# Kernel optimization log

Hardware: AMD Instinct MI355X
Metric: run time of the kernel (lower is better)

## Reference

```python
import jax, jax.numpy as jnp
import numpy as np

TOP_K = 2
EPS = 1e-6

def setup_inputs() -> dict:
    key = jax.random.key(0)
    ks = jax.random.split(key, 6)
    Bt, S, D, E, R = 4, 4096, 1024, 8, 4
    s = lambda d: 1.0 / np.sqrt(d)
    return {
        "x": jax.random.normal(ks[0], (Bt, S, D), jnp.float32),
        "W_base": jax.random.normal(ks[1], (D, D), jnp.float32) * s(D),
        "b_base": jax.random.normal(ks[2], (D,), jnp.float32) * 0.02,
        "W_router": jax.random.normal(ks[3], (E, D), jnp.float32) * s(D),
        "A": jax.random.normal(ks[4], (E, D, R), jnp.float32) * s(D),
        "B": jax.random.normal(ks[5], (E, R, D), jnp.float32) * s(R),
    }

def reference(x, W_base, b_base, W_router, A, B):
    # frozen base linear: [b,s,d] @ [out,d]^T + bias
    base_out = jnp.einsum('bsd,od->bso', x, W_base) + b_base
    # router softmax gate over experts
    logits = jnp.einsum('bsd,ed->bse', x, W_router)
    gate = jax.nn.softmax(logits, axis=-1)
    # top-k scatter-mask (values kept are the gate values themselves)
    topv, topi = jax.lax.top_k(gate, TOP_K)                    # [b,s,k]
    mask = jnp.sum(jax.nn.one_hot(topi, gate.shape[-1], dtype=gate.dtype), axis=-2)
    gate = gate * mask
    gate = gate / (jnp.sum(gate, axis=-1, keepdims=True) + EPS)
    # batched rank-4 LoRA experts, gating applied in low-rank space
    h = jnp.einsum('bsd,edr->bser', x, A)                      # [b,s,E,r]
    hg = h * gate[..., None]                                   # weight before up-proj
    lora_out = jnp.einsum('bser,ero->bso', hg, B)
    return base_out + lora_out
```

## Files before the change

kernel.cpp:

```cpp
#include <hip/hip_runtime.h>
#include <cstdint>

typedef __attribute__((ext_vector_type(8))) short short8;
typedef __attribute__((ext_vector_type(4))) float f32x4;

__device__ inline unsigned short f2bf(float f){
  union { float f; uint32_t u; } v; v.f = f;
  uint32_t r = v.u + 0x7FFFu + ((v.u >> 16) & 1u);
  return (unsigned short)(r >> 16);
}

#define GLL(gp, lp) __builtin_amdgcn_global_load_lds(              \
    (const __attribute__((address_space(1))) void*)(gp),           \
    (__attribute__((address_space(3))) void*)(lp), 16, 0, 0)

#define DSRO(dst, addr, off) \
  asm volatile("ds_read_b128 %0, %1 offset:" off : "=v"(dst) : "v"(addr))

__global__ __launch_bounds__(256) void kconv(const float* __restrict__ W,
                                             const float* __restrict__ A,
                                             const float* __restrict__ Bm,
                                             unsigned short* __restrict__ Wb,
                                             unsigned short* __restrict__ BTt,
                                             unsigned short* __restrict__ W2b){
  int i = blockIdx.x * 256 + threadIdx.x;
  Wb[i] = f2bf(W[i]);
  if (i < 32768){
    int o = i >> 5, c = i & 31;
    BTt[i] = f2bf(Bm[(size_t)c*1024 + o]);
    int n = i >> 10, d = i & 1023;
    W2b[i] = f2bf(A[(((size_t)(n>>2))*1024 + d)*4 + (n&3)]);
  }
}

__global__ __launch_bounds__(256) void kxl2(const float* __restrict__ x,
                                            const float* __restrict__ Wr,
                                            unsigned short* __restrict__ xb,
                                            float* __restrict__ gate){
  __shared__ float wr[8192];
  const int tid  = threadIdx.x;
  const int lane = tid & 63;
  const int wid  = tid >> 6;
  {
    const float4* s  = (const float4*)Wr;
    float4*       d4 = (float4*)wr;
    #pragma unroll
    for (int j=0;j<8;j++) d4[j*256+tid] = s[j*256+tid];
  }
  __syncthreads();
  const int tk  = lane >> 3, ln8 = lane & 7;
  const size_t tok = (size_t)blockIdx.x*32 + wid*8 + tk;
  const float4* xr = (const float4*)(x + tok*1024);
  ushort4*      xd = (ushort4*)(xb + tok*1024);
  const float4* wv = (const float4*)wr;
  float p[8] = {0.f,0.f,0.f,0.f,0.f,0.f,0.f,0.f};
  #pragma unroll 4
  for (int it=0; it<32; it++){
    float4 v = xr[it*8 + ln8];
    ushort4 o; o.x=f2bf(v.x); o.y=f2bf(v.y); o.z=f2bf(v.z); o.w=f2bf(v.w);
    xd[it*8 + ln8] = o;
    #pragma unroll
    for (int e=0;e<8;e++){
      float4 wq = wv[e*256 + it*8 + ln8];
      p[e] += v.x*wq.x + v.y*wq.y + v.z*wq.z + v.w*wq.w;
    }
  }
  #pragma unroll
  for (int off=1; off<8; off<<=1){
    #pragma unroll
    for (int e=0;e<8;e++) p[e] += __shfl_xor(p[e], off, 64);
  }
  if (ln8 == 0){
    float mx = p[0];
    #pragma unroll
    for (int e=1;e<8;e++) mx = fmaxf(mx, p[e]);
    float ex[8], s2 = 0.f;
    #pragma unroll
    for (int e=0;e<8;e++){ ex[e] = __expf(p[e]-mx); s2 += ex[e]; }
    int i1 = 0; float v1 = ex[0];
    #pragma unroll
    for (int e=1;e<8;e++) if (ex[e] > v1){ v1 = ex[e]; i1 = e; }
    int i2 = -1; float v2 = -1.f;
    #pragma unroll
    for (int e=0;e<8;e++) if (e != i1 && ex[e] > v2){ v2 = ex[e]; i2 = e; }
    float g1 = v1/s2, g2 = v2/s2;
    float rs = 1.f/(g1 + g2 + 1e-6f);
    float* go = gate + tok*8;
    #pragma unroll
    for (int e=0;e<8;e++) go[e] = (e==i1 ? g1 : (e==i2 ? g2 : 0.f)) * rs;
  }
}

__global__ __launch_bounds__(512, 2) void kgemm6(const unsigned short* __restrict__ xb,
                                                 const unsigned short* __restrict__ Wb,
                                                 const unsigned short* __restrict__ BTt,
                                                 const unsigned short* __restrict__ W2b,
                                                 const float* __restrict__ gate,
                                                 const float* __restrict__ bias,
                                                 float* __restrict__ out){
  __shared__ __attribute__((aligned(128))) char lds[131072];
  char* ldsc = lds;
  const uint32_t L = (uint32_t)(uintptr_t)lds;
  const int tid  = threadIdx.x;
  const int lane = tid & 63;
  const int w    = tid >> 6;
  const int mblk = blockIdx.x & 63;
  const int nblk = blockIdx.x >> 6;
  const int m0 = mblk << 8, n0 = nblk << 8;
  const int wm = w >> 2, wn = w & 3;
  const int lrow = lane & 15;
  const int q    = lane >> 4;

  const int swzk = (lrow & 7) << 4;
  const uint32_t vA0 = L + (uint32_t)(wm*128 + lrow)*128 + (uint32_t)((q<<4) ^ swzk);
  const uint32_t vA1 = L + (uint32_t)(wm*128 + lrow)*128 + (uint32_t)(((q^4)<<4) ^ swzk);
  const uint32_t vB0 = L + 65536u + (uint32_t)(wn*64 + lrow)*128 + (uint32_t)((q<<4) ^ swzk);
  const uint32_t vB1 = L + 65536u + (uint32_t)(wn*64 + lrow)*128 + (uint32_t)(((q^4)<<4) ^ swzk);

  const int rowL = lane >> 3;
  const int colb = ((lane & 7) ^ rowL) << 4;
  const int rbA = (w>>2)*128 + (w&3)*16;
  const int rbB = (w>>1)*64 + (w&1)*16;
  const char* Ag = (const char*)xb + ((size_t)(m0 + rbA + rowL) << 11) + colb;
  const char* Bg = (const char*)Wb + ((size_t)(n0 + rbB + rowL) << 11) + colb;

#define STG_A(tt, h, ss) do{                                                    \
    GLL(Ag + (size_t)(h)*131072 + (tt)*128,                                     \
        ldsc + (ss)*32768 + (rbA + (h)*64)*128 + lane*16);                      \
    GLL(Ag + (size_t)(h)*131072 + 16384 + (tt)*128,                             \
        ldsc + (ss)*32768 + (rbA + (h)*64 + 8)*128 + lane*16); }while(0)
#define STG_B(tt, h, ss) do{                                                    \
    GLL(Bg + (size_t)(h)*65536 + (tt)*128,                                      \
        ldsc + 65536 + (ss)*32768 + (rbB + (h)*32)*128 + lane*16);              \
    GLL(Bg + (size_t)(h)*65536 + 16384 + (tt)*128,                              \
        ldsc + 65536 + (ss)*32768 + (rbB + (h)*32 + 8)*128 + lane*16); }while(0)

  f32x4 acc[8][4];
  #pragma unroll
  for (int a2=0;a2<8;a2++)
    #pragma unroll
    for (int b2=0;b2<4;b2++) acc[a2][b2] = (f32x4){0.f,0.f,0.f,0.f};
  f32x4 acc_h[4];
  #pragma unroll
  for (int f=0; f<4; f++) acc_h[f] = (f32x4){0.f,0.f,0.f,0.f};

  const unsigned short* c2p = W2b + (size_t)((wn&1)*16 + lrow)*1024 + q*8;

  STG_A(0,0,0); STG_A(0,1,0); STG_B(0,0,0); STG_B(0,1,0);
  asm volatile("s_waitcnt vmcnt(0)" ::: "memory");
  __builtin_amdgcn_s_barrier();

  short8 a[8], b0[4], b1[4];
  #pragma unroll 1
  for (int t = 0; t < 16; ++t){
    const int s = t & 1, sn = s ^ 1;
    const uint32_t va0 = vA0 + s*32768, va1 = vA1 + s*32768;
    const uint32_t vb0 = vB0 + s*32768, vb1 = vB1 + s*32768;
    short8 c2[2];
    c2[0] = *(const short8*)(c2p + t*64);
    c2[1] = *(const short8*)(c2p + t*64 + 32);
    DSRO(a[0], va0, "0");    DSRO(a[1], va1, "0");
    DSRO(a[2], va0, "2048"); DSRO(a[3], va1, "2048");
    DSRO(a[4], va0, "4096"); DSRO(a[5], va1, "4096");
    DSRO(a[6], va0, "6144"); DSRO(a[7], va1, "6144");
    DSRO(b0[0], vb0, "0");    DSRO(b0[1], vb1, "0");
    DSRO(b0[2], vb0, "2048"); DSRO(b0[3], vb1, "2048");
    if (t < 15){ STG_A(t+1, 0, sn); asm volatile("s_waitcnt vmcnt(2)" ::: "memory"); }
    else       {                    asm volatile("s_waitcnt vmcnt(0)" ::: "memory"); }
    __builtin_amdgcn_s_barrier();
    asm volatile("s_waitcnt lgkmcnt(0)" ::: "memory");
    __builtin_amdgcn_sched_barrier(0);
    __builtin_amdgcn_s_setprio(1);
    #pragma unroll
    for (int kk=0;kk<2;kk++)
      #pragma unroll
      for (int fm=0;fm<4;fm++)
        #pragma unroll
        for (int fn=0;fn<2;fn++)
          acc[fm][fn] = __builtin_amdgcn_mfma_f32_16x16x32_bf16(a[fm*2+kk], b0[fn*2+kk], acc[fm][fn], 0, 0, 0);
    __builtin_amdgcn_s_setprio(0);
    __builtin_amdgcn_s_barrier();
    DSRO(b1[0], vb0, "4096"); DSRO(b1[1], vb1, "4096");
    DSRO(b1[2], vb0, "6144"); DSRO(b1[3], vb1, "6144");
    if (t < 15) STG_A(t+1, 1, sn);
    __builtin_amdgcn_s_barrier();
    asm volatile("s_waitcnt lgkmcnt(0)" ::: "memory");
    __builtin_amdgcn_sched_barrier(0);
    __builtin_amdgcn_s_setprio(1);
    #pragma unroll
    for (int kk=0;kk<2;kk++)
      #pragma unroll
      for (int fm=0;fm<4;fm++)
        #pragma unroll
        for (int fn=0;fn<2;fn++)
          acc[fm][2+fn] = __builtin_amdgcn_mfma_f32_16x16x32_bf16(a[fm*2+kk], b1[fn*2+kk], acc[fm][2+fn], 0, 0, 0);
    if (wn < 2){
      #pragma unroll
      for (int kk=0;kk<2;kk++)
        #pragma unroll
        for (int f=0;f<4;f++)
          acc_h[f] = __builtin_amdgcn_mfma_f32_16x16x32_bf16(a[f*2+kk], c2[kk], acc_h[f], 0, 0, 0);
    }
    __builtin_amdgcn_s_setprio(0);
    __builtin_amdgcn_s_barrier();
    DSRO(a[0], va0, "8192");  DSRO(a[1], va1, "8192");
    DSRO(a[2], va0, "10240"); DSRO(a[3], va1, "10240");
    DSRO(a[4], va0, "12288"); DSRO(a[5], va1, "12288");
    DSRO(a[6], va0, "14336"); DSRO(a[7], va1, "14336");
    if (t < 15) STG_B(t+1, 0, sn);
    __builtin_amdgcn_s_barrier();
    asm volatile("s_waitcnt lgkmcnt(0)" ::: "memory");
    __builtin_amdgcn_sched_barrier(0);
    __builtin_amdgcn_s_setprio(1);
    #pragma unroll
    for (int kk=0;kk<2;kk++)
      #pragma unroll
      for (int fm=0;fm<4;fm++)
        #pragma unroll
        for (int fn=0;fn<2;fn++)
          acc[4+fm][2+fn] = __builtin_amdgcn_mfma_f32_16x16x32_bf16(a[fm*2+kk], b1[fn*2+kk], acc[4+fm][2+fn], 0, 0, 0);
    __builtin_amdgcn_s_setprio(0);
    __builtin_amdgcn_s_barrier();
    if (t < 15){ STG_B(t+1, 1, sn); asm volatile("s_waitcnt vmcnt(2)" ::: "memory"); }
    __builtin_amdgcn_s_barrier();
    __builtin_amdgcn_s_setprio(1);
    #pragma unroll
    for (int kk=0;kk<2;kk++)
      #pragma unroll
      for (int fm=0;fm<4;fm++)
        #pragma unroll
        for (int fn=0;fn<2;fn++)
          acc[4+fm][fn] = __builtin_amdgcn_mfma_f32_16x16x32_bf16(a[fm*2+kk], b0[fn*2+kk], acc[4+fm][fn], 0, 0, 0);
    if (wn >= 2){
      #pragma unroll
      for (int kk=0;kk<2;kk++)
        #pragma unroll
        for (int f=0;f<4;f++)
          acc_h[f] = __builtin_amdgcn_mfma_f32_16x16x32_bf16(a[f*2+kk], c2[kk], acc_h[f], 0, 0, 0);
    }
    __builtin_amdgcn_s_setprio(0);
    __builtin_amdgcn_s_barrier();
  }

  __syncthreads();
  {
    float4* gl4 = (float4*)(ldsc + 24576);
    gl4[tid] = ((const float4*)(gate + (size_t)m0*8))[tid];
  }
  __syncthreads();
  unsigned short* HGl = (unsigned short*)ldsc;
  const float*    gl  = (const float*)(ldsc + 24576);
  {
    const int rbase = wm*128 + (wn>>1)*64;
    const int n = (wn&1)*16 + lrow;
    #pragma unroll
    for (int f=0; f<4; f++)
      #pragma unroll
      for (int j=0;j<4;j++){
        int row = rbase + f*16 + q*4 + j;
        HGl[row*40 + n] = f2bf(acc_h[f][j] * gl[row*8 + (n>>2)]);
      }
  }
  __syncthreads();
  {
    short8 hb[4];
    #pragma unroll
    for (int fn=0; fn<4; fn++)
      hb[fn] = *(const short8*)(BTt + (size_t)(n0 + wn*64 + fn*16 + lrow)*32 + q*8);
    #pragma unroll
    for (int fm=0; fm<8; fm++){
      short8 ha = *(const short8*)((const char*)HGl + (size_t)(wm*128 + fm*16 + lrow)*80 + q*16);
      #pragma unroll
      for (int fn=0; fn<4; fn++)
        acc[fm][fn] = __builtin_amdgcn_mfma_f32_16x16x32_bf16(ha, hb[fn], acc[fm][fn], 0, 0, 0);
    }
  }

  #pragma unroll
  for (int fn=0;fn<4;fn++){
    int col = n0 + wn*64 + fn*16 + lrow;
    float bv = bias[col];
    #pragma unroll
    for (int fm=0;fm<8;fm++){
      int rb = m0 + wm*128 + fm*16 + q*4;
      #pragma unroll
      for (int j=0;j<4;j++)
        out[(size_t)(rb+j)*1024 + col] = acc[fm][fn][j] + bv;
    }
  }
#undef STG_A
#undef STG_B
}

extern "C" void kernel_launch(void* const* d_in, const int* in_sizes, int n_in,
                              void* d_out, int out_size, void* d_ws, size_t ws_size,
                              hipStream_t stream){
  const float* x  = (const float*)d_in[0];
  const float* W  = (const float*)d_in[1];
  const float* bb = (const float*)d_in[2];
  const float* Wr = (const float*)d_in[3];
  const float* A  = (const float*)d_in[4];
  const float* Bm = (const float*)d_in[5];
  float* out = (float*)d_out;
  char* ws = (char*)d_ws;

  unsigned short* Wb   = (unsigned short*)(ws + 0);
  unsigned short* BTt  = (unsigned short*)(ws + 2097152);
  unsigned short* W2b  = (unsigned short*)(ws + 2162688);
  float*          gate = (float*)         (ws + 2228224);
  unsigned short* xb   = (unsigned short*)(ws + 2752512);

  kconv<<<4096, 256, 0, stream>>>(W, A, Bm, Wb, BTt, W2b);
  kxl2<<<512, 256, 0, stream>>>(x, Wr, xb, gate);
  kgemm6<<<256, 512, 0, stream>>>(xb, Wb, BTt, W2b, gate, bb, out);
}
```

Measured before the change: 86.85 us.

## Prefetch LoRA down-projection fragments and overlap LDS reads with MFMA sub-phases

Replaces the synchronous per-iteration global loads of the LoRA A fragments (c2) with asm global loads issued one K-step ahead and double-buffered in registers. Each MFMA phase is split in half with a partial lgkmcnt wait, so the first MFMAs start while later ds_reads are still in flight. The vmcnt waits are adjusted to account for the extra outstanding loads. It also shrinks the LDS row stride for the gated hidden tile from 40 to 36 elements and moves the gate buffer to match. The finer waits and hand-written vmcnt counts make the schedule fragile, and the new stride could change LDS bank-conflict behaviour.

New measurement: 82.01 us. -5.6%, faster.

```diff
diff --git a/kernel.cpp b/kernel.cpp
--- a/kernel.cpp
+++ b/kernel.cpp
@@ -16,6 +16,8 @@
 
 #define DSRO(dst, addr, off) \
   asm volatile("ds_read_b128 %0, %1 offset:" off : "=v"(dst) : "v"(addr))
+#define GLD16(dst, ptr) \
+  asm volatile("global_load_dwordx4 %0, %1, off" : "=v"(dst) : "v"(ptr) : "memory")
 
 __global__ __launch_bounds__(256) void kconv(const float* __restrict__ W,
                                              const float* __restrict__ A,
@@ -145,9 +147,13 @@
   for (int f=0; f<4; f++) acc_h[f] = (f32x4){0.f,0.f,0.f,0.f};
 
   const unsigned short* c2p = W2b + (size_t)((wn&1)*16 + lrow)*1024 + q*8;
+  short8 c2cur0, c2cur1, c2nxt0, c2nxt1;
 
   STG_A(0,0,0); STG_A(0,1,0); STG_B(0,0,0); STG_B(0,1,0);
+  GLD16(c2cur0, c2p);
+  GLD16(c2cur1, c2p + 32);
   asm volatile("s_waitcnt vmcnt(0)" ::: "memory");
+  __builtin_amdgcn_sched_barrier(0);
   __builtin_amdgcn_s_barrier();
 
   short8 a[8], b0[4], b1[4];
@@ -156,50 +162,62 @@
     const int s = t & 1, sn = s ^ 1;
     const uint32_t va0 = vA0 + s*32768, va1 = vA1 + s*32768;
     const uint32_t vb0 = vB0 + s*32768, vb1 = vB1 + s*32768;
-    short8 c2[2];
-    c2[0] = *(const short8*)(c2p + t*64);
-    c2[1] = *(const short8*)(c2p + t*64 + 32);
     DSRO(a[0], va0, "0");    DSRO(a[1], va1, "0");
     DSRO(a[2], va0, "2048"); DSRO(a[3], va1, "2048");
     DSRO(a[4], va0, "4096"); DSRO(a[5], va1, "4096");
     DSRO(a[6], va0, "6144"); DSRO(a[7], va1, "6144");
+    if (t < 15){ STG_A(t+1, 0, sn); asm volatile("s_waitcnt vmcnt(2)" ::: "memory"); }
+    else       {                    asm volatile("s_waitcnt vmcnt(0)" ::: "memory"); }
+    __builtin_amdgcn_sched_barrier(0);
     DSRO(b0[0], vb0, "0");    DSRO(b0[1], vb1, "0");
     DSRO(b0[2], vb0, "2048"); DSRO(b0[3], vb1, "2048");
-    if (t < 15){ STG_A(t+1, 0, sn); asm volatile("s_waitcnt vmcnt(2)" ::: "memory"); }
-    else       {                    asm volatile("s_waitcnt vmcnt(0)" ::: "memory"); }
-    __builtin_amdgcn_s_barrier();
+    __builtin_amdgcn_s_barrier();
+    asm volatile("s_waitcnt lgkmcnt(2)" ::: "memory");
+    __builtin_amdgcn_sched_barrier(0);
+    __builtin_amdgcn_s_setprio(1);
+    #pragma unroll
+    for (int kk=0;kk<2;kk++)
+      #pragma unroll
+      for (int fm=0;fm<4;fm++)
+        acc[fm][0] = __builtin_amdgcn_mfma_f32_16x16x32_bf16(a[fm*2+kk], b0[kk], acc[fm][0], 0, 0, 0);
     asm volatile("s_waitcnt lgkmcnt(0)" ::: "memory");
     __builtin_amdgcn_sched_barrier(0);
-    __builtin_amdgcn_s_setprio(1);
-    #pragma unroll
-    for (int kk=0;kk<2;kk++)
-      #pragma unroll
-      for (int fm=0;fm<4;fm++)
-        #pragma unroll
-        for (int fn=0;fn<2;fn++)
-          acc[fm][fn] = __builtin_amdgcn_mfma_f32_16x16x32_bf16(a[fm*2+kk], b0[fn*2+kk], acc[fm][fn], 0, 0, 0);
+    #pragma unroll
+    for (int kk=0;kk<2;kk++)
+      #pragma unroll
+      for (int fm=0;fm<4;fm++)
+        acc[fm][1] = __builtin_amdgcn_mfma_f32_16x16x32_bf16(a[fm*2+kk], b0[2+kk], acc[fm][1], 0, 0, 0);
     __builtin_amdgcn_s_setprio(0);
     __builtin_amdgcn_s_barrier();
     DSRO(b1[0], vb0, "4096"); DSRO(b1[1], vb1, "4096");
     DSRO(b1[2], vb0, "6144"); DSRO(b1[3], vb1, "6144");
-    if (t < 15) STG_A(t+1, 1, sn);
-    __builtin_amdgcn_s_barrier();
+    if (t < 15){
+      STG_A(t+1, 1, sn);
+      GLD16(c2nxt0, c2p + (t+1)*64);
+      GLD16(c2nxt1, c2p + (t+1)*64 + 32);
+    }
+    __builtin_amdgcn_s_barrier();
+    asm volatile("s_waitcnt lgkmcnt(2)" ::: "memory");
+    __builtin_amdgcn_sched_barrier(0);
+    __builtin_amdgcn_s_setprio(1);
+    #pragma unroll
+    for (int kk=0;kk<2;kk++)
+      #pragma unroll
+      for (int fm=0;fm<4;fm++)
+        acc[fm][2] = __builtin_amdgcn_mfma_f32_16x16x32_bf16(a[fm*2+kk], b1[kk], acc[fm][2], 0, 0, 0);
     asm volatile("s_waitcnt lgkmcnt(0)" ::: "memory");
     __builtin_amdgcn_sched_barrier(0);
-    __builtin_amdgcn_s_setprio(1);
-    #pragma unroll
-    for (int kk=0;kk<2;kk++)
-      #pragma unroll
-      for (int fm=0;fm<4;fm++)
-        #pragma unroll
-        for (int fn=0;fn<2;fn++)
-          acc[fm][2+fn] = __builtin_amdgcn_mfma_f32_16x16x32_bf16(a[fm*2+kk], b1[fn*2+kk], acc[fm][2+fn], 0, 0, 0);
+    #pragma unroll
+    for (int kk=0;kk<2;kk++)
+      #pragma unroll
+      for (int fm=0;fm<4;fm++)
+        acc[fm][3] = __builtin_amdgcn_mfma_f32_16x16x32_bf16(a[fm*2+kk], b1[2+kk], acc[fm][3], 0, 0, 0);
     if (wn < 2){
       #pragma unroll
-      for (int kk=0;kk<2;kk++)
-        #pragma unroll
-        for (int f=0;f<4;f++)
-          acc_h[f] = __builtin_amdgcn_mfma_f32_16x16x32_bf16(a[f*2+kk], c2[kk], acc_h[f], 0, 0, 0);
+      for (int f=0;f<4;f++){
+        acc_h[f] = __builtin_amdgcn_mfma_f32_16x16x32_bf16(a[f*2],   c2cur0, acc_h[f], 0, 0, 0);
+        acc_h[f] = __builtin_amdgcn_mfma_f32_16x16x32_bf16(a[f*2+1], c2cur1, acc_h[f], 0, 0, 0);
+      }
     }
     __builtin_amdgcn_s_setprio(0);
     __builtin_amdgcn_s_barrier();
@@ -209,19 +227,32 @@
     DSRO(a[6], va0, "14336"); DSRO(a[7], va1, "14336");
     if (t < 15) STG_B(t+1, 0, sn);
     __builtin_amdgcn_s_barrier();
+    asm volatile("s_waitcnt lgkmcnt(4)" ::: "memory");
+    __builtin_amdgcn_sched_barrier(0);
+    __builtin_amdgcn_s_setprio(1);
+    #pragma unroll
+    for (int kk=0;kk<2;kk++)
+      #pragma unroll
+      for (int fm=0;fm<2;fm++)
+        #pragma unroll
+        for (int fn=0;fn<2;fn++)
+          acc[4+fm][2+fn] = __builtin_amdgcn_mfma_f32_16x16x32_bf16(a[fm*2+kk], b1[fn*2+kk], acc[4+fm][2+fn], 0, 0, 0);
     asm volatile("s_waitcnt lgkmcnt(0)" ::: "memory");
     __builtin_amdgcn_sched_barrier(0);
-    __builtin_amdgcn_s_setprio(1);
-    #pragma unroll
-    for (int kk=0;kk<2;kk++)
-      #pragma unroll
-      for (int fm=0;fm<4;fm++)
+    #pragma unroll
+    for (int kk=0;kk<2;kk++)
+      #pragma unroll
+      for (int fm=2;fm<4;fm++)
         #pragma unroll
         for (int fn=0;fn<2;fn++)
           acc[4+fm][2+fn] = __builtin_amdgcn_mfma_f32_16x16x32_bf16(a[fm*2+kk], b1[fn*2+kk], acc[4+fm][2+fn], 0, 0, 0);
     __builtin_amdgcn_s_setprio(0);
     __builtin_amdgcn_s_barrier();
-    if (t < 15){ STG_B(t+1, 1, sn); asm volatile("s_waitcnt vmcnt(2)" ::: "memory"); }
+    if (t < 15){
+      STG_B(t+1, 1, sn);
+      asm volatile("s_waitcnt vmcnt(4)" ::: "memory");
+    }
+    __builtin_amdgcn_sched_barrier(0);
     __builtin_amdgcn_s_barrier();
     __builtin_amdgcn_s_setprio(1);
     #pragma unroll
@@ -233,23 +264,24 @@
           acc[4+fm][fn] = __builtin_amdgcn_mfma_f32_16x16x32_bf16(a[fm*2+kk], b0[fn*2+kk], acc[4+fm][fn], 0, 0, 0);
     if (wn >= 2){
       #pragma unroll
-      for (int kk=0;kk<2;kk++)
-        #pragma unroll
-        for (int f=0;f<4;f++)
-          acc_h[f] = __builtin_amdgcn_mfma_f32_16x16x32_bf16(a[f*2+kk], c2[kk], acc_h[f], 0, 0, 0);
+      for (int f=0;f<4;f++){
+        acc_h[f] = __builtin_amdgcn_mfma_f32_16x16x32_bf16(a[f*2],   c2cur0, acc_h[f], 0, 0, 0);
+        acc_h[f] = __builtin_amdgcn_mfma_f32_16x16x32_bf16(a[f*2+1], c2cur1, acc_h[f], 0, 0, 0);
+      }
     }
     __builtin_amdgcn_s_setprio(0);
     __builtin_amdgcn_s_barrier();
+    c2cur0 = c2nxt0; c2cur1 = c2nxt1;
   }
 
   __syncthreads();
   {
-    float4* gl4 = (float4*)(ldsc + 24576);
+    float4* gl4 = (float4*)(ldsc + 20480);
     gl4[tid] = ((const float4*)(gate + (size_t)m0*8))[tid];
   }
   __syncthreads();
   unsigned short* HGl = (unsigned short*)ldsc;
-  const float*    gl  = (const float*)(ldsc + 24576);
+  const float*    gl  = (const float*)(ldsc + 20480);
   {
     const int rbase = wm*128 + (wn>>1)*64;
     const int n = (wn&1)*16 + lrow;
@@ -258,7 +290,7 @@
       #pragma unroll
       for (int j=0;j<4;j++){
         int row = rbase + f*16 + q*4 + j;
-        HGl[row*40 + n] = f2bf(acc_h[f][j] * gl[row*8 + (n>>2)]);
+        HGl[row*36 + n] = f2bf(acc_h[f][j] * gl[row*8 + (n>>2)]);
       }
   }
   __syncthreads();
@@ -269,7 +301,7 @@
       hb[fn] = *(const short8*)(BTt + (size_t)(n0 + wn*64 + fn*16 + lrow)*32 + q*8);
     #pragma unroll
     for (int fm=0; fm<8; fm++){
-      short8 ha = *(const short8*)((const char*)HGl + (size_t)(wm*128 + fm*16 + lrow)*80 + q*16);
+      short8 ha = *(const short8*)((const char*)HGl + (size_t)(wm*128 + fm*16 + lrow)*72 + q*16);
       #pragma unroll
       for (int fn=0; fn<4; fn++)
         acc[fm][fn] = __builtin_amdgcn_mfma_f32_16x16x32_bf16(ha, hb[fn], acc[fm][fn], 0, 0, 0);
```
